# Kernel tuning notes

Hardware: AMD Instinct MI355X
Metric: run time of the kernel (lower is better)

Reference implementation:

```python
import jax, jax.numpy as jnp
import numpy as np

N_NODES = 100000
N_EDGES = 1600000
C_IN = 128
C_OUT = 128
BN_EPS = 1e-5
LEAKY_SLOPE = 0.01


def setup_inputs() -> dict:
    key = jax.random.key(0)
    k1, k2, k3 = jax.random.split(key, 3)
    x = jax.random.normal(k1, (N_NODES, C_IN), dtype=jnp.float32)
    edge_index = jax.random.randint(k2, (2, N_EDGES), 0, N_NODES, dtype=jnp.int64)
    # GCNConv linear weight (glorot-ish scale) and bias
    W = jax.random.normal(k3, (C_IN, C_OUT), dtype=jnp.float32) * (1.0 / np.sqrt(C_IN))
    bias = jnp.zeros((C_OUT,), dtype=jnp.float32)
    # BatchNorm affine params
    gamma = jnp.ones((C_OUT,), dtype=jnp.float32)
    beta = jnp.zeros((C_OUT,), dtype=jnp.float32)
    return {"x": x, "edge_index": edge_index, "W": W, "bias": bias,
            "gamma": gamma, "beta": beta}


def reference(x, edge_index, W, bias, gamma, beta):
    N = x.shape[0]
    # --- GCNConv (add self loops, symmetric degree normalization) ---
    loop = jnp.arange(N, dtype=edge_index.dtype)
    src = jnp.concatenate([edge_index[0], loop])  # message sources (x_j)
    dst = jnp.concatenate([edge_index[1], loop])  # aggregation targets
    ones = jnp.ones(src.shape[0], dtype=x.dtype)
    deg = jax.ops.segment_sum(ones, dst, num_segments=N)
    dinv_sqrt = jnp.where(deg > 0, jax.lax.rsqrt(deg), 0.0).astype(x.dtype)
    norm = dinv_sqrt[src] * dinv_sqrt[dst]  # [E+N]

    h = x @ W                                # [N, C_out], transform first
    msg = h[src] * norm[:, None]             # gather + edge weighting
    out = jax.ops.segment_sum(msg, dst, num_segments=N) + bias  # scatter-add

    # --- LeakyReLU ---
    out = jax.nn.leaky_relu(out, negative_slope=LEAKY_SLOPE)

    # --- BatchNorm over nodes (training-mode batch stats, biased var) ---
    mean = out.mean(axis=0)
    var = out.var(axis=0)
    out = (out - mean) * jax.lax.rsqrt(var + BN_EPS) * gamma + beta
    return out
```

## Files before the change

### kernel.cpp

```cpp
#include <hip/hip_runtime.h>

#define N_NODES 100000
#define N_EDGES 1600000
#define C 128
#define LEAKY 0.01f
#define BN_EPS 1e-5f
#define NB_C 391
#define PB 391
#define PBLK 4096
#define STASH 8192
#define NBG 1563
#define NAGG 6250
#define NRED 64

typedef __attribute__((ext_vector_type(8))) short short8;
typedef __attribute__((ext_vector_type(4))) float f32x4;

__device__ __forceinline__ unsigned short f2bf(float f) {
    unsigned int u = __builtin_bit_cast(unsigned int, f);
    u += 0x7FFFu + ((u >> 16) & 1u);
    return (unsigned short)(u >> 16);
}
__device__ __forceinline__ float bf2f(unsigned short b) {
    unsigned int u = ((unsigned int)b) << 16;
    return __builtin_bit_cast(float, u);
}

__global__ __launch_bounds__(256) void k_init(const float* __restrict__ W,
                                              unsigned short* __restrict__ wt,
                                              unsigned short* __restrict__ hs) {
    int i = blockIdx.x * 256 + threadIdx.x;
    wt[i] = f2bf(W[(i & 127) * C + (i >> 7)]);
    if (i < C) hs[(size_t)N_NODES * C + i] = 0;
}

__global__ __launch_bounds__(256) void k_coarse(const int* __restrict__ dst,
                                                int* __restrict__ blk_cnt) {
    __shared__ int lh[NB_C];
    int tid = threadIdx.x, blk = blockIdx.x;
    for (int i = tid; i < NB_C; i += 256) lh[i] = 0;
    __syncthreads();
    #pragma unroll
    for (int it = 0; it < PBLK / 256; ++it) {
        int e = blk * PBLK + it * 256 + tid;
        if (e < N_EDGES) atomicAdd(&lh[dst[e] >> 8], 1);
    }
    __syncthreads();
    for (int i = tid; i < NB_C; i += 256) blk_cnt[i * PB + blk] = lh[i];
}

__global__ __launch_bounds__(512) void k_offsets(const int* __restrict__ blk_cnt,
                                                 int* __restrict__ offset,
                                                 int* __restrict__ total) {
    __shared__ int tmp[512];
    int t = threadIdx.x, k = blockIdx.x;
    int v = (t < PB) ? blk_cnt[k * PB + t] : 0;
    tmp[t] = v;
    __syncthreads();
    for (int off = 1; off < 512; off <<= 1) {
        int u = (t >= off) ? tmp[t - off] : 0;
        __syncthreads();
        tmp[t] += u;
        __syncthreads();
    }
    if (t < PB) offset[k * PB + t] = tmp[t] - v;
    if (t == 511) total[k] = tmp[511];
}

__global__ __launch_bounds__(512) void k_cbase(const int* __restrict__ total,
                                               int* __restrict__ cbase,
                                               int* __restrict__ offs) {
    __shared__ int tmp[512];
    int t = threadIdx.x;
    int v = (t < NB_C) ? total[t] : 0;
    tmp[t] = v;
    __syncthreads();
    for (int off = 1; off < 512; off <<= 1) {
        int u = (t >= off) ? tmp[t - off] : 0;
        __syncthreads();
        tmp[t] += u;
        __syncthreads();
    }
    if (t < NB_C) cbase[t] = tmp[t] - v;
    if (t == 0) { cbase[NB_C] = N_EDGES; offs[N_NODES] = N_EDGES; }
}

__global__ __launch_bounds__(256) void k_partition(const int* __restrict__ src,
                                                   const int* __restrict__ dst,
                                                   const int* __restrict__ cbase,
                                                   const int* __restrict__ offset,
                                                   unsigned int* __restrict__ pairs) {
    __shared__ int lh[NB_C];
    __shared__ int lbase[NB_C];
    int tid = threadIdx.x, blk = blockIdx.x;
    for (int i = tid; i < NB_C; i += 256) {
        lh[i] = 0;
        lbase[i] = cbase[i] + offset[i * PB + blk];
    }
    __syncthreads();
    #pragma unroll
    for (int it = 0; it < PBLK / 256; ++it) {
        int e = blk * PBLK + it * 256 + tid;
        if (e < N_EDGES) {
            int d = dst[e];
            int b = d >> 8;
            int r = atomicAdd(&lh[b], 1);
            pairs[lbase[b] + r] = (unsigned int)src[e] | ((unsigned int)(d & 255) << 17);
        }
    }
}

__global__ __launch_bounds__(256) void k_fine(const unsigned int* __restrict__ pairs,
                                              const int* __restrict__ cbase,
                                              float* __restrict__ dinv,
                                              int* __restrict__ offs,
                                              int* __restrict__ srt) {
    __shared__ int hist[256];
    __shared__ int loff[256];
    __shared__ int cnt2[256];
    __shared__ unsigned int stash[STASH];
    int tid = threadIdx.x, blk = blockIdx.x;
    int nbase = blk * 256;
    int nn = (nbase + 256 <= N_NODES) ? 256 : (N_NODES - nbase);
    int ebeg = cbase[blk];
    int ne = cbase[blk + 1] - ebeg;

    hist[tid] = 0; cnt2[tid] = 0;
    __syncthreads();
    for (int k = tid; k < ne; k += 256) {
        unsigned int pk = pairs[ebeg + k];
        if (k < STASH) stash[k] = pk;
        atomicAdd(&hist[pk >> 17], 1);
    }
    __syncthreads();
    if (tid < nn) dinv[nbase + tid] = rsqrtf((float)(hist[tid] + 1));
    loff[tid] = hist[tid];
    __syncthreads();
    for (int off = 1; off < 256; off <<= 1) {
        int u = (tid >= off) ? loff[tid - off] : 0;
        __syncthreads();
        loff[tid] += u;
        __syncthreads();
    }
    loff[tid] -= hist[tid];
    if (tid < nn) offs[nbase + tid] = ebeg + loff[tid];
    __syncthreads();
    for (int k = tid; k < ne; k += 256) {
        unsigned int pk = (k < STASH) ? stash[k] : pairs[ebeg + k];
        int dl = pk >> 17;
        int r = atomicAdd(&cnt2[dl], 1);
        srt[ebeg + loff[dl] + r] = (int)(pk & 0x1FFFFu);
    }
}

__global__ __launch_bounds__(256) void k_gemm_hs(const float* __restrict__ x,
                                                 const unsigned short* __restrict__ wt,
                                                 const float* __restrict__ dinv,
                                                 unsigned short* __restrict__ hs) {
    int tile = blockIdx.x * 4 + (threadIdx.x >> 6);
    if (tile >= N_NODES / 16) return;
    int lane = threadIdx.x & 63;
    int row0 = tile * 16;
    int ar = lane & 15;
    int kg = (lane >> 4) * 8;

    short8 a[4];
    #pragma unroll
    for (int kk = 0; kk < 4; ++kk) {
        const float* p = &x[(size_t)(row0 + ar) * C + kk * 32 + kg];
        float4 p0 = *(const float4*)p;
        float4 p1 = *(const float4*)(p + 4);
        short8 av;
        av[0] = (short)f2bf(p0.x); av[1] = (short)f2bf(p0.y);
        av[2] = (short)f2bf(p0.z); av[3] = (short)f2bf(p0.w);
        av[4] = (short)f2bf(p1.x); av[5] = (short)f2bf(p1.y);
        av[6] = (short)f2bf(p1.z); av[7] = (short)f2bf(p1.w);
        a[kk] = av;
    }

    int rb = (lane >> 4) * 4;
    float dv[4];
    #pragma unroll
    for (int r = 0; r < 4; ++r) dv[r] = dinv[row0 + rb + r];

    #pragma unroll
    for (int ct = 0; ct < 8; ++ct) {
        f32x4 acc = {0.f, 0.f, 0.f, 0.f};
        #pragma unroll
        for (int kk = 0; kk < 4; ++kk) {
            short8 b = *(const short8*)&wt[(size_t)(ct * 16 + ar) * C + kk * 32 + kg];
            acc = __builtin_amdgcn_mfma_f32_16x16x32_bf16(a[kk], b, acc, 0, 0, 0);
        }
        int col = ct * 16 + ar;
        #pragma unroll
        for (int r = 0; r < 4; ++r)
            hs[(size_t)(row0 + rb + r) * C + col] = f2bf(acc[r] * dv[r]);
    }
}

__global__ __launch_bounds__(256) void k_aggregate(const short8* __restrict__ hs8,
                                                   const int* __restrict__ srt,
                                                   const int* __restrict__ offs,
                                                   const float* __restrict__ dinv,
                                                   const float* __restrict__ bias,
                                                   short8* __restrict__ vb8,
                                                   float* __restrict__ part) {
    __shared__ float lsv[16][C + 4];
    int tid = threadIdx.x;
    int g = tid >> 4, c8 = tid & 15;
    int node = blockIdx.x * 16 + g;

    float dn = dinv[node];
    int beg = offs[node];
    int end = offs[node + 1];

    short8 ms = hs8[(size_t)node * 16 + c8];
    float ax[8];
    #pragma unroll
    for (int ch = 0; ch < 8; ++ch) ax[ch] = bf2f((unsigned short)ms[ch]);

    for (int k = beg; k < end; k += 8) {
        int idx[8];
        #pragma unroll
        for (int i = 0; i < 8; ++i) {
            int ki = k + i;
            idx[i] = (ki < end) ? srt[ki] : N_NODES;
        }
        short8 m[8];
        #pragma unroll
        for (int i = 0; i < 8; ++i) m[i] = hs8[(size_t)idx[i] * 16 + c8];
        #pragma unroll
        for (int i = 0; i < 8; ++i)
            #pragma unroll
            for (int ch = 0; ch < 8; ++ch)
                ax[ch] += bf2f((unsigned short)m[i][ch]);
    }

    float4 b0 = *(const float4*)&bias[c8 * 8];
    float4 b1 = *(const float4*)&bias[c8 * 8 + 4];
    float bb[8] = {b0.x, b0.y, b0.z, b0.w, b1.x, b1.y, b1.z, b1.w};

    short8 o;
    #pragma unroll
    for (int ch = 0; ch < 8; ++ch) {
        float v = dn * ax[ch] + bb[ch];
        v = v > 0.0f ? v : LEAKY * v;
        o[ch] = (short)f2bf(v);
        lsv[g][c8 * 8 + ch] = v;
    }
    vb8[(size_t)node * 16 + c8] = o;

    __syncthreads();
    if (tid < C) {
        float s = 0.0f, q = 0.0f;
        #pragma unroll
        for (int g2 = 0; g2 < 16; ++g2) {
            float t = lsv[g2][tid];
            s += t; q += t * t;
        }
        part[(size_t)blockIdx.x * 256 + tid]     = s;
        part[(size_t)blockIdx.x * 256 + C + tid] = q;
    }
}

__global__ __launch_bounds__(256) void k_reduce(const float* __restrict__ part,
                                                float* __restrict__ part2) {
    int t = threadIdx.x, b = blockIdx.x;
    float s = 0.0f;
    for (int r = b; r < NAGG; r += NRED) s += part[(size_t)r * 256 + t];
    part2[(size_t)b * 256 + t] = s;
}

__global__ __launch_bounds__(256) void k_params(const float* __restrict__ part2,
                                                const float* __restrict__ gamma,
                                                const float* __restrict__ beta,
                                                float* __restrict__ scale,
                                                float* __restrict__ shift) {
    __shared__ float tot[256];
    int t = threadIdx.x;
    float s = 0.0f;
    #pragma unroll
    for (int b = 0; b < NRED; ++b) s += part2[(size_t)b * 256 + t];
    tot[t] = s;
    __syncthreads();
    if (t < C) {
        float inv_n = 1.0f / (float)N_NODES;
        float mean = tot[t] * inv_n;
        float var = tot[C + t] * inv_n - mean * mean;
        float sc = gamma[t] * rsqrtf(var + BN_EPS);
        scale[t] = sc;
        shift[t] = beta[t] - mean * sc;
    }
}

__global__ __launch_bounds__(256) void k_apply(const short8* __restrict__ vb8,
                                               const float* __restrict__ scale,
                                               const float* __restrict__ shift,
                                               float* __restrict__ out) {
    int i = blockIdx.x * 256 + threadIdx.x;
    int c8 = i & 15;
    short8 v = vb8[i];
    float4 sc0 = *(const float4*)&scale[c8 * 8];
    float4 sc1 = *(const float4*)&scale[c8 * 8 + 4];
    float4 sh0 = *(const float4*)&shift[c8 * 8];
    float4 sh1 = *(const float4*)&shift[c8 * 8 + 4];
    float4 o0, o1;
    o0.x = bf2f((unsigned short)v[0]) * sc0.x + sh0.x;
    o0.y = bf2f((unsigned short)v[1]) * sc0.y + sh0.y;
    o0.z = bf2f((unsigned short)v[2]) * sc0.z + sh0.z;
    o0.w = bf2f((unsigned short)v[3]) * sc0.w + sh0.w;
    o1.x = bf2f((unsigned short)v[4]) * sc1.x + sh1.x;
    o1.y = bf2f((unsigned short)v[5]) * sc1.y + sh1.y;
    o1.z = bf2f((unsigned short)v[6]) * sc1.z + sh1.z;
    o1.w = bf2f((unsigned short)v[7]) * sc1.w + sh1.w;
    float4* op = (float4*)out + (size_t)i * 2;
    op[0] = o0;
    op[1] = o1;
}

extern "C" void kernel_launch(void* const* d_in, const int* in_sizes, int n_in,
                              void* d_out, int out_size, void* d_ws, size_t ws_size,
                              hipStream_t stream) {
    const float* x     = (const float*)d_in[0];
    const int*   edge  = (const int*)d_in[1];
    const float* W     = (const float*)d_in[2];
    const float* bias  = (const float*)d_in[3];
    const float* gamma = (const float*)d_in[4];
    const float* beta  = (const float*)d_in[5];
    float* out = (float*)d_out;
    char* ws = (char*)d_ws;

    unsigned short* hs    = (unsigned short*)ws;  ws += (size_t)(N_NODES + 1) * C * 2;
    unsigned short* vb    = (unsigned short*)ws;  ws += (size_t)N_NODES * C * 2;
    unsigned short* wt    = (unsigned short*)ws;  ws += (size_t)C * C * 2;
    unsigned int*   pairs = (unsigned int*)ws;    ws += (size_t)N_EDGES * 4;
    int*   srt     = (int*)ws;                    ws += (size_t)N_EDGES * 4;
    int*   blk_cnt = (int*)ws;                    ws += (size_t)NB_C * PB * 4;
    int*   offset  = (int*)ws;                    ws += (size_t)NB_C * PB * 4;
    int*   total   = (int*)ws;                    ws += 512 * 4;
    int*   cbase   = (int*)ws;                    ws += 512 * 4;
    int*   offs    = (int*)ws;                    ws += (size_t)(N_NODES + 1) * 4;
    float* dinv    = (float*)ws;                  ws += (size_t)N_NODES * 4;
    float* part2   = (float*)ws;                  ws += (size_t)NRED * 256 * 4;
    float* scale   = (float*)ws;                  ws += C * 4;
    float* shift   = (float*)ws;

    float* part = (float*)pairs;

    const int* src = edge;
    const int* dst = edge + N_EDGES;

    k_init     <<<C * C / 256,           256, 0, stream>>>(W, wt, hs);
    k_coarse   <<<PB,                    256, 0, stream>>>(dst, blk_cnt);
    k_offsets  <<<NB_C,                  512, 0, stream>>>(blk_cnt, offset, total);
    k_cbase    <<<1,                     512, 0, stream>>>(total, cbase, offs);
    k_partition<<<PB,                    256, 0, stream>>>(src, dst, cbase, offset, pairs);
    k_fine     <<<NB_C,                  256, 0, stream>>>(pairs, cbase, dinv, offs, srt);
    k_gemm_hs  <<<NBG,                   256, 0, stream>>>(x, wt, dinv, hs);
    k_aggregate<<<NAGG,                  256, 0, stream>>>((const short8*)hs, srt, offs, dinv, bias, (short8*)vb, part);
    k_reduce   <<<NRED,                  256, 0, stream>>>(part, part2);
    k_params   <<<1,                     256, 0, stream>>>(part2, gamma, beta, scale, shift);
    k_apply    <<<N_NODES * C / 8 / 256, 256, 0, stream>>>((const short8*)vb, scale, shift, out);
}
```

Before: 194.6 us.

## Aggregate one node per wavefront with 32-bit lanes; fold weight init into coarse

The aggregation kernel is restructured so each wavefront handles one node at a time, four nodes in sequence, with each lane loading a 4-byte pair of bf16 channels. Before, 16 threads shared a node and each did 16-byte gathers. The node index is uniform across the wavefront, so edge indices and loop bounds are scalar and there is no divergence across nodes of different degree. The per-block statistics reduction now accumulates in registers and sums four wave partials instead of scanning a 16-row shared tile. Separately, the weight transpose/convert and padding-row zeroing move into k_coarse, removing one kernel launch. The trade-off is smaller gather transactions per lane, which may lower memory-level parallelism.

After: 189.5 us, median of 3. 1.03x faster.

```diff
diff --git a/kernel.cpp b/kernel.cpp
--- a/kernel.cpp
+++ b/kernel.cpp
@@ -26,18 +26,16 @@
     return __builtin_bit_cast(float, u);
 }
 
-__global__ __launch_bounds__(256) void k_init(const float* __restrict__ W,
-                                              unsigned short* __restrict__ wt,
-                                              unsigned short* __restrict__ hs) {
-    int i = blockIdx.x * 256 + threadIdx.x;
-    wt[i] = f2bf(W[(i & 127) * C + (i >> 7)]);
-    if (i < C) hs[(size_t)N_NODES * C + i] = 0;
-}
-
 __global__ __launch_bounds__(256) void k_coarse(const int* __restrict__ dst,
-                                                int* __restrict__ blk_cnt) {
+                                                int* __restrict__ blk_cnt,
+                                                const float* __restrict__ W,
+                                                unsigned short* __restrict__ wt,
+                                                unsigned short* __restrict__ hs) {
     __shared__ int lh[NB_C];
     int tid = threadIdx.x, blk = blockIdx.x;
+    int gi = blk * 256 + tid;
+    if (gi < C * C) wt[gi] = f2bf(W[(gi & 127) * C + (gi >> 7)]);
+    if (gi < C) hs[(size_t)N_NODES * C + gi] = 0;
     for (int i = tid; i < NB_C; i += 256) lh[i] = 0;
     __syncthreads();
     #pragma unroll
@@ -198,68 +196,66 @@
     }
 }
 
-__global__ __launch_bounds__(256) void k_aggregate(const short8* __restrict__ hs8,
+__global__ __launch_bounds__(256) void k_aggregate(const unsigned int* __restrict__ hs32,
                                                    const int* __restrict__ srt,
                                                    const int* __restrict__ offs,
                                                    const float* __restrict__ dinv,
                                                    const float* __restrict__ bias,
-                                                   short8* __restrict__ vb8,
+                                                   unsigned int* __restrict__ vb32,
                                                    float* __restrict__ part) {
-    __shared__ float lsv[16][C + 4];
+    __shared__ float red_s[4][C];
+    __shared__ float red_q[4][C];
+    int wave = threadIdx.x >> 6, lane = threadIdx.x & 63;
+    float2 bb = ((const float2*)bias)[lane];
+    float s0 = 0.f, s1 = 0.f, q0 = 0.f, q1 = 0.f;
+
+    #pragma unroll
+    for (int g = 0; g < 4; ++g) {
+        int node = __builtin_amdgcn_readfirstlane(blockIdx.x * 16 + g * 4 + wave);
+        float dn = dinv[node];
+        int beg = offs[node];
+        int end = offs[node + 1];
+
+        unsigned int ms = hs32[(size_t)node * 64 + lane];
+        float ax0 = __builtin_bit_cast(float, ms << 16);
+        float ax1 = __builtin_bit_cast(float, ms & 0xFFFF0000u);
+
+        for (int k = beg; k < end; k += 8) {
+            int idx[8];
+            #pragma unroll
+            for (int i = 0; i < 8; ++i) {
+                int ki = k + i;
+                idx[i] = (ki < end) ? srt[ki] : N_NODES;
+            }
+            unsigned int m[8];
+            #pragma unroll
+            for (int i = 0; i < 8; ++i) m[i] = hs32[(size_t)idx[i] * 64 + lane];
+            #pragma unroll
+            for (int i = 0; i < 8; ++i) {
+                ax0 += __builtin_bit_cast(float, m[i] << 16);
+                ax1 += __builtin_bit_cast(float, m[i] & 0xFFFF0000u);
+            }
+        }
+
+        float v0 = dn * ax0 + bb.x; v0 = v0 > 0.f ? v0 : LEAKY * v0;
+        float v1 = dn * ax1 + bb.y; v1 = v1 > 0.f ? v1 : LEAKY * v1;
+        vb32[(size_t)node * 64 + lane] =
+            (unsigned int)f2bf(v0) | ((unsigned int)f2bf(v1) << 16);
+        s0 += v0; q0 += v0 * v0;
+        s1 += v1; q1 += v1 * v1;
+    }
+
+    red_s[wave][lane * 2] = s0;  red_s[wave][lane * 2 + 1] = s1;
+    red_q[wave][lane * 2] = q0;  red_q[wave][lane * 2 + 1] = q1;
+    __syncthreads();
     int tid = threadIdx.x;
-    int g = tid >> 4, c8 = tid & 15;
-    int node = blockIdx.x * 16 + g;
-
-    float dn = dinv[node];
-    int beg = offs[node];
-    int end = offs[node + 1];
-
-    short8 ms = hs8[(size_t)node * 16 + c8];
-    float ax[8];
-    #pragma unroll
-    for (int ch = 0; ch < 8; ++ch) ax[ch] = bf2f((unsigned short)ms[ch]);
-
-    for (int k = beg; k < end; k += 8) {
-        int idx[8];
-        #pragma unroll
-        for (int i = 0; i < 8; ++i) {
-            int ki = k + i;
-            idx[i] = (ki < end) ? srt[ki] : N_NODES;
-        }
-        short8 m[8];
-        #pragma unroll
-        for (int i = 0; i < 8; ++i) m[i] = hs8[(size_t)idx[i] * 16 + c8];
-        #pragma unroll
-        for (int i = 0; i < 8; ++i)
-            #pragma unroll
-            for (int ch = 0; ch < 8; ++ch)
-                ax[ch] += bf2f((unsigned short)m[i][ch]);
-    }
-
-    float4 b0 = *(const float4*)&bias[c8 * 8];
-    float4 b1 = *(const float4*)&bias[c8 * 8 + 4];
-    float bb[8] = {b0.x, b0.y, b0.z, b0.w, b1.x, b1.y, b1.z, b1.w};
-
-    short8 o;
-    #pragma unroll
-    for (int ch = 0; ch < 8; ++ch) {
-        float v = dn * ax[ch] + bb[ch];
-        v = v > 0.0f ? v : LEAKY * v;
-        o[ch] = (short)f2bf(v);
-        lsv[g][c8 * 8 + ch] = v;
-    }
-    vb8[(size_t)node * 16 + c8] = o;
-
-    __syncthreads();
     if (tid < C) {
-        float s = 0.0f, q = 0.0f;
-        #pragma unroll
-        for (int g2 = 0; g2 < 16; ++g2) {
-            float t = lsv[g2][tid];
-            s += t; q += t * t;
-        }
-        part[(size_t)blockIdx.x * 256 + tid]     = s;
-        part[(size_t)blockIdx.x * 256 + C + tid] = q;
+        part[(size_t)blockIdx.x * 256 + tid] =
+            red_s[0][tid] + red_s[1][tid] + red_s[2][tid] + red_s[3][tid];
+    } else {
+        int c = tid - C;
+        part[(size_t)blockIdx.x * 256 + tid] =
+            red_q[0][c] + red_q[1][c] + red_q[2][c] + red_q[3][c];
     }
 }
 
@@ -350,14 +346,14 @@
     const int* src = edge;
     const int* dst = edge + N_EDGES;
 
-    k_init     <<<C * C / 256,           256, 0, stream>>>(W, wt, hs);
-    k_coarse   <<<PB,                    256, 0, stream>>>(dst, blk_cnt);
+    k_coarse   <<<PB,                    256, 0, stream>>>(dst, blk_cnt, W, wt, hs);
     k_offsets  <<<NB_C,                  512, 0, stream>>>(blk_cnt, offset, total);
     k_cbase    <<<1,                     512, 0, stream>>>(total, cbase, offs);
     k_partition<<<PB,                    256, 0, stream>>>(src, dst, cbase, offset, pairs);
     k_fine     <<<NB_C,                  256, 0, stream>>>(pairs, cbase, dinv, offs, srt);
     k_gemm_hs  <<<NBG,                   256, 0, stream>>>(x, wt, dinv, hs);
-    k_aggregate<<<NAGG,                  256, 0, stream>>>((const short8*)hs, srt, offs, dinv, bias, (short8*)vb, part);
+    k_aggregate<<<NAGG,                  256, 0, stream>>>((const unsigned int*)hs, srt, offs, dinv, bias,
+                                                           (unsigned int*)vb, part);
     k_reduce   <<<NRED,                  256, 0, stream>>>(part, part2);
     k_params   <<<1,                     256, 0, stream>>>(part2, gamma, beta, scale, shift);
     k_apply    <<<N_NODES * C / 8 / 256, 256, 0, stream>>>((const short8*)vb, scale, shift, out);
```
